# Kernel tuning notes

Hardware: AMD Instinct MI355X
Metric: run time of the kernel (lower is better)

Reference implementation:

```python
import jax, jax.numpy as jnp
import numpy as np

B, N, K = 4, 4096, 16
DP, DM = 128, 512


def _gather(points, idx):
    # points [B,N,C], idx [B,N,K] -> [B,N,K,C] (index_points)
    b, n, k = idx.shape
    flat = jnp.take_along_axis(points, idx.reshape(b, -1)[:, :, None], axis=1)
    return flat.reshape(b, n, k, points.shape[-1])


def _mlp2(x, w1, b1, w2, b2):
    return jax.nn.relu(x @ w1 + b1) @ w2 + b2


def setup_inputs():
    key = jax.random.key(0)
    ks = jax.random.split(key, 20)
    s_dp = 1.0 / np.sqrt(DP)
    s_dm = 1.0 / np.sqrt(DM)
    return {
        "xyz": jax.random.normal(ks[0], (B, N, 3), jnp.float32),
        "features": jax.random.normal(ks[1], (B, N, DP), jnp.float32),
        "fc1_w": jax.random.normal(ks[2], (DP, DM), jnp.float32) * s_dp,
        "fc1_b": jnp.zeros((DM,), jnp.float32),
        "fc2_w": jax.random.normal(ks[3], (DM, DP), jnp.float32) * s_dm,
        "fc2_b": jnp.zeros((DP,), jnp.float32),
        "wq": jax.random.normal(ks[4], (DM, DM), jnp.float32) * s_dm,
        "wk": jax.random.normal(ks[5], (DM, DM), jnp.float32) * s_dm,
        "wv": jax.random.normal(ks[6], (DM, DM), jnp.float32) * s_dm,
        "d1_w": jax.random.normal(ks[7], (3, DM), jnp.float32) * (1.0 / np.sqrt(3.0)),
        "d1_b": jnp.zeros((DM,), jnp.float32),
        "d2_w": jax.random.normal(ks[8], (DM, DM), jnp.float32) * s_dm,
        "d2_b": jnp.zeros((DM,), jnp.float32),
        "g1_w": jax.random.normal(ks[9], (DM, DM), jnp.float32) * s_dm,
        "g1_b": jnp.zeros((DM,), jnp.float32),
        "g2_w": jax.random.normal(ks[10], (DM, DM), jnp.float32) * s_dm,
        "g2_b": jnp.zeros((DM,), jnp.float32),
    }


def reference(xyz, features, fc1_w, fc1_b, fc2_w, fc2_b, wq, wk, wv,
              d1_w, d1_b, d2_w, d2_b, g1_w, g1_b, g2_w, g2_b):
    # square_distance via ||a-b||^2 = |a|^2 + |b|^2 - 2 a.b  (avoids [B,N,N,3])
    sq = jnp.sum(xyz * xyz, axis=-1)                       # [B,N]
    dists = sq[:, :, None] + sq[:, None, :] - 2.0 * jnp.einsum('bnc,bmc->bnm', xyz, xyz)
    knn_idx = jax.lax.top_k(-dists, K)[1]                  # [B,N,K] k-nearest
    knn_xyz = _gather(xyz, knn_idx)                        # [B,N,K,3]

    pre = features
    x = features @ fc1_w + fc1_b                           # [B,N,DM]
    q = x @ wq                                             # [B,N,DM]
    k = _gather(x @ wk, knn_idx)                           # [B,N,K,DM]
    v = _gather(x @ wv, knn_idx)                           # [B,N,K,DM]

    pos_enc = _mlp2(xyz[:, :, None] - knn_xyz, d1_w, d1_b, d2_w, d2_b)  # [B,N,K,DM]
    attn = _mlp2(q[:, :, None] - k + pos_enc, g1_w, g1_b, g2_w, g2_b)   # [B,N,K,DM]
    attn = jax.nn.softmax(attn / np.sqrt(DM), axis=-2)     # softmax over neighbors
    res = jnp.sum(attn * (v + pos_enc), axis=2)            # einsum bmnf,bmnf->bmf
    res = res @ fc2_w + fc2_b + pre                        # [B,N,DP]
    return res, attn
```

## Files before the change

### kernel.cpp

```cpp
#include <hip/hip_runtime.h>

#define NPTS   4096
#define NBATCH 4
#define KNN    16
#define DMODEL 512
#define DPOINT 128
#define QKVLD  1536

#define BN 128
#define BK 64

typedef unsigned short bfu;
typedef __attribute__((ext_vector_type(8))) short short8;
typedef __attribute__((ext_vector_type(4))) float f32x4;

__device__ __forceinline__ bfu f2bf(float f) {
    unsigned u = __builtin_bit_cast(unsigned, f);
    return (bfu)((u + 0x7fffu + ((u >> 16) & 1u)) >> 16);
}
__device__ __forceinline__ float bf2f(bfu h) {
    unsigned u = ((unsigned)h) << 16;
    return __builtin_bit_cast(float, u);
}

__device__ __forceinline__ void gload_lds16(const bfu* g, bfu* l) {
    __builtin_amdgcn_global_load_lds(
        (const __attribute__((address_space(1))) void*)g,
        (__attribute__((address_space(3))) void*)l, 16, 0, 0);
}

#define TPQ 8
#define QPB 32

__device__ __forceinline__ void knn_merge_level(float* bd, int* bi, int lvl)
{
    float pd[KNN]; int pi[KNN];
#pragma unroll
    for (int i = 0; i < KNN; ++i) {
        pd[i] = __shfl_xor(bd[KNN-1-i], lvl);
        pi[i] = __shfl_xor(bi[KNN-1-i], lvl);
    }
#pragma unroll
    for (int i = 0; i < KNN; ++i) {
        bool take = (pd[i] < bd[i]) || (pd[i] == bd[i] && pi[i] < bi[i]);
        if (take) { bd[i] = pd[i]; bi[i] = pi[i]; }
    }
#pragma unroll
    for (int s = 8; s >= 1; s >>= 1) {
#pragma unroll
        for (int i = 0; i < KNN; ++i) {
            if ((i & s) == 0) {
                const int j = i + s;
                bool sw = (bd[j] < bd[i]) || (bd[j] == bd[i] && bi[j] < bi[i]);
                if (sw) {
                    float td = bd[i]; bd[i] = bd[j]; bd[j] = td;
                    int   ti = bi[i]; bi[i] = bi[j]; bi[j] = ti;
                }
            }
        }
    }
}

__global__ __launch_bounds__(256) void knn_kernel(const float* __restrict__ xyz,
                                                  int* __restrict__ knn_out)
{
    __shared__ float4 pts[NPTS];
    const int b    = blockIdx.y;
    const int tid  = threadIdx.x;
    const int qloc = tid >> 3;
    const int sub  = tid & 7;
    const int n    = blockIdx.x * QPB + qloc;

    const float* bx = xyz + (size_t)b * NPTS * 3;
    for (int i = tid; i < NPTS; i += 256) {
        float x = bx[i*3+0], y = bx[i*3+1], z = bx[i*3+2];
        pts[i] = make_float4(x, y, z, x*x + y*y + z*z);
    }
    __syncthreads();

    const float4 me = pts[n];
    float bd[KNN];
    int   bi[KNN];
#pragma unroll
    for (int i = 0; i < KNN; ++i) { bd[i] = 3.4e38f; bi[i] = -1; }

    for (int t0 = 0; t0 < NPTS / TPQ; t0 += 8) {
        float d[8];
#pragma unroll
        for (int j = 0; j < 8; ++j) {
            float4 o = pts[sub + ((t0 + j) << 3)];
            d[j] = me.w + o.w - 2.f*(me.x*o.x + me.y*o.y + me.z*o.z);
        }
        float mn = fminf(fminf(fminf(d[0],d[1]),fminf(d[2],d[3])),
                         fminf(fminf(d[4],d[5]),fminf(d[6],d[7])));
        if (mn < bd[KNN-1]) {
#pragma unroll
            for (int j = 0; j < 8; ++j) {
                float dj = d[j];
                if (dj < bd[KNN-1]) {
                    const int m = sub + ((t0 + j) << 3);
#pragma unroll
                    for (int i = KNN-1; i >= 1; --i) {
                        float dp = bd[i-1];
                        if (dp > dj)        { bd[i] = dp; bi[i] = bi[i-1]; }
                        else if (bd[i] > dj){ bd[i] = dj; bi[i] = m; }
                    }
                    if (bd[0] > dj) { bd[0] = dj; bi[0] = m; }
                }
            }
        }
    }

    knn_merge_level(bd, bi, 1);
    knn_merge_level(bd, bi, 2);
    knn_merge_level(bd, bi, 4);

    int* orow = knn_out + ((size_t)b*NPTS + n) * KNN;
    const int base = b * NPTS;
    orow[sub*2+0] = base + bi[sub*2+0];
    orow[sub*2+1] = base + bi[sub*2+1];
}

__global__ __launch_bounds__(256) void prep_weights(
    const float* __restrict__ fc1_w, const float* __restrict__ wq,
    const float* __restrict__ wk,    const float* __restrict__ wv,
    const float* __restrict__ d2_w,  const float* __restrict__ g1_w,
    const float* __restrict__ g2_w,  const float* __restrict__ fc2_w,
    bfu* __restrict__ fc1T, bfu* __restrict__ qkvT, bfu* __restrict__ d2T,
    bfu* __restrict__ g1T,  bfu* __restrict__ g2T,  bfu* __restrict__ fc2T)
{
    int i = blockIdx.x * 256 + threadIdx.x;
    const int S1 = DPOINT * DMODEL;
    const int S2 = DMODEL * DMODEL;
    if (i < S1) { fc1T[i] = f2bf(fc1_w[(size_t)(i & 127) * DMODEL + (i >> 7)]); return; }
    i -= S1;
    if (i < S2) { qkvT[i]        = f2bf(wq[(size_t)(i & 511) * DMODEL + (i >> 9)]); return; }
    i -= S2;
    if (i < S2) { qkvT[S2 + i]   = f2bf(wk[(size_t)(i & 511) * DMODEL + (i >> 9)]); return; }
    i -= S2;
    if (i < S2) { qkvT[2*S2 + i] = f2bf(wv[(size_t)(i & 511) * DMODEL + (i >> 9)]); return; }
    i -= S2;
    if (i < S2) { d2T[i] = f2bf(d2_w[(size_t)(i & 511) * DMODEL + (i >> 9)]); return; }
    i -= S2;
    if (i < S2) { g1T[i] = f2bf(g1_w[(size_t)(i & 511) * DMODEL + (i >> 9)]); return; }
    i -= S2;
    if (i < S2) { g2T[i] = f2bf(g2_w[(size_t)(i & 511) * DMODEL + (i >> 9)]); return; }
    i -= S2;
    if (i < S1) { fc2T[i] = f2bf(fc2_w[(size_t)(i & 511) * DPOINT + (i >> 9)]); return; }
}

__global__ __launch_bounds__(256) void cvt_bf16(const float* __restrict__ src,
                                                bfu* __restrict__ dst, int n4)
{
    int i = blockIdx.x * 256 + threadIdx.x;
    if (i < n4) {
        float4 v = ((const float4*)src)[i];
        bfu* d = dst + (size_t)i * 4;
        d[0] = f2bf(v.x); d[1] = f2bf(v.y); d[2] = f2bf(v.z); d[3] = f2bf(v.w);
    }
}

__global__ __launch_bounds__(256) void pos_h_kernel(
    const float* __restrict__ xyz, const int* __restrict__ knng,
    const float* __restrict__ d1w, const float* __restrict__ d1b,
    bfu* __restrict__ out, int row_base)
{
    const int idx  = blockIdx.x * 256 + threadIdx.x;
    const int rloc = idx >> 6;
    const int c0   = (idx & 63) * 8;
    const int grow = row_base + rloc;
    const int p    = grow >> 4;
    const int nb   = knng[grow];
    const float rx = xyz[(size_t)p*3+0] - xyz[(size_t)nb*3+0];
    const float ry = xyz[(size_t)p*3+1] - xyz[(size_t)nb*3+1];
    const float rz = xyz[(size_t)p*3+2] - xyz[(size_t)nb*3+2];
    short8 ov;
#pragma unroll
    for (int j = 0; j < 8; ++j) {
        const int k = c0 + j;
        float v = d1b[k];
        v = fmaf(rx, d1w[k],        v);
        v = fmaf(ry, d1w[512 + k],  v);
        v = fmaf(rz, d1w[1024 + k], v);
        ov[j] = (short)f2bf(fmaxf(v, 0.f));
    }
    *(short8*)&out[(size_t)rloc * DMODEL + c0] = ov;
}

template<int BMt, bool BIAS, bool RELU, bool OUTBF, bool RESID, bool AIN, bool SMAX>
__global__ __launch_bounds__(256) void gemm_mfma(
    const bfu* __restrict__ A, const bfu* __restrict__ BT,
    const float* __restrict__ bias, const float* __restrict__ resid,
    void* __restrict__ Cout, int M, int Kd, int Nd,
    const int* __restrict__ knng,
    const bfu* __restrict__ qb, const bfu* __restrict__ kb,
    const bfu* __restrict__ posc, const bfu* __restrict__ vb,
    bfu* __restrict__ auxb, int row_base)
{
    constexpr int MF  = BMt / 32;
    constexpr int RPW = BMt / 4;

    __shared__ bfu As[BMt * BK];
    __shared__ bfu Bs[BN * BK];

    const int tid  = threadIdx.x;
    const int lane = tid & 63;
    const int w    = tid >> 6;

    const int nbn     = Nd / BN;
    const int q8      = gridDim.x >> 3;
    const int logical = (blockIdx.x & 7) * q8 + (blockIdx.x >> 3);
    const int bm      = (logical / nbn) * BMt;
    const int bn      = (logical % nbn) * BN;

    const int wm   = (w >> 1) * (BMt / 2);
    const int wn   = (w & 1) * 64;
    const int lrow = lane & 15;
    const int kgrp = lane >> 4;

    f32x4 acc[MF][4];
#pragma unroll
    for (int m = 0; m < MF; ++m)
#pragma unroll
        for (int n = 0; n < 4; ++n) acc[m][n] = (f32x4){0.f, 0.f, 0.f, 0.f};

    for (int k0 = 0; k0 < Kd; k0 += BK) {
        __syncthreads();

        {
            int r0 = w * 32;
            const bfu* gB = BT + (size_t)(bn + r0 + (lane >> 3)) * Kd + k0 + (lane & 7) * 8;
            bfu* lB = Bs + r0 * BK;
#pragma unroll
            for (int i = 0; i < 4; ++i)
                gload_lds16(gB + (size_t)i * 8 * Kd, lB + i * 8 * BK);
        }
        {
            int r0 = w * RPW;
            const bfu* gA = A + (size_t)(bm + r0 + (lane >> 3)) * Kd + k0 + (lane & 7) * 8;
            bfu* lA = As + r0 * BK;
#pragma unroll
            for (int i = 0; i < RPW / 8; ++i)
                gload_lds16(gA + (size_t)i * 8 * Kd, lA + i * 8 * BK);
        }

        __syncthreads();

#pragma unroll
        for (int kk = 0; kk < BK; kk += 32) {
            short8 af[MF], bfr[4];
#pragma unroll
            for (int m = 0; m < MF; ++m)
                af[m] = *(const short8*)&As[(wm + m * 16 + lrow) * BK + kk + kgrp * 8];
#pragma unroll
            for (int n = 0; n < 4; ++n)
                bfr[n] = *(const short8*)&Bs[(wn + n * 16 + lrow) * BK + kk + kgrp * 8];
#pragma unroll
            for (int m = 0; m < MF; ++m)
#pragma unroll
                for (int n = 0; n < 4; ++n)
                    acc[m][n] = __builtin_amdgcn_mfma_f32_16x16x32_bf16(
                        af[m], bfr[n], acc[m][n], 0, 0, 0);
        }
    }

    if constexpr (AIN) {
#pragma unroll
        for (int m = 0; m < MF; ++m) {
            const int row0 = bm + wm + m * 16 + kgrp * 4;
            int p4[4], g4[4];
#pragma unroll
            for (int r = 0; r < 4; ++r) {
                const int grow = row_base + row0 + r;
                p4[r] = grow >> 4;
                g4[r] = knng[grow];
            }
#pragma unroll
            for (int n = 0; n < 4; ++n) {
                const int col = bn + wn + n * 16 + lrow;
                const float bv = bias[col];
#pragma unroll
                for (int r = 0; r < 4; ++r) {
                    const size_t o = (size_t)(row0 + r) * DMODEL + col;
                    bfu pb = f2bf(acc[m][n][r] + bv);
                    ((bfu*)Cout)[o] = pb;
                    float qv = bf2f(qb[(size_t)p4[r] * QKVLD + col]);
                    float kv = bf2f(kb[(size_t)g4[r] * QKVLD + col]);
                    auxb[o] = f2bf(qv - kv + bf2f(pb));
                }
            }
        }
        return;
    }

    if constexpr (SMAX) {
        const float scale = 0.044194173824159216f;
#pragma unroll
        for (int m = 0; m < MF; ++m) {
            const int row0 = bm + wm + m * 16 + kgrp * 4;
            const int ploc = (bm + wm + m * 16) >> 4;
            int gnb4[4];
#pragma unroll
            for (int r = 0; r < 4; ++r) gnb4[r] = knng[(size_t)row_base + row0 + r];
#pragma unroll
            for (int n = 0; n < 4; ++n) {
                const int col = bn + wn + n * 16 + lrow;
                const float bv = bias[col];
                float v0 = (acc[m][n][0] + bv) * scale;
                float v1 = (acc[m][n][1] + bv) * scale;
                float v2 = (acc[m][n][2] + bv) * scale;
                float v3 = (acc[m][n][3] + bv) * scale;
                float mx = fmaxf(fmaxf(v0, v1), fmaxf(v2, v3));
                mx = fmaxf(mx, __shfl_xor(mx, 16));
                mx = fmaxf(mx, __shfl_xor(mx, 32));
                float e0 = __expf(v0 - mx), e1 = __expf(v1 - mx);
                float e2 = __expf(v2 - mx), e3 = __expf(v3 - mx);
                float s = e0 + e1 + e2 + e3;
                s += __shfl_xor(s, 16);
                s += __shfl_xor(s, 32);
                const float inv = 1.f / s;
                float a0 = e0*inv, a1 = e1*inv, a2 = e2*inv, a3 = e3*inv;
                float* ao = (float*)Cout;
                ao[(size_t)(row0 + 0) * DMODEL + col] = a0;
                ao[(size_t)(row0 + 1) * DMODEL + col] = a1;
                ao[(size_t)(row0 + 2) * DMODEL + col] = a2;
                ao[(size_t)(row0 + 3) * DMODEL + col] = a3;
                float res = 0.f;
                res = fmaf(a0, bf2f(vb[(size_t)gnb4[0]*QKVLD + col]) + bf2f(posc[(size_t)(row0+0)*DMODEL + col]), res);
                res = fmaf(a1, bf2f(vb[(size_t)gnb4[1]*QKVLD + col]) + bf2f(posc[(size_t)(row0+1)*DMODEL + col]), res);
                res = fmaf(a2, bf2f(vb[(size_t)gnb4[2]*QKVLD + col]) + bf2f(posc[(size_t)(row0+2)*DMODEL + col]), res);
                res = fmaf(a3, bf2f(vb[(size_t)gnb4[3]*QKVLD + col]) + bf2f(posc[(size_t)(row0+3)*DMODEL + col]), res);
                res += __shfl_xor(res, 16);
                res += __shfl_xor(res, 32);
                if (kgrp == 0) {
                    const size_t pglob = (size_t)(row_base >> 4) + ploc;
                    auxb[pglob * DMODEL + col] = f2bf(res);
                }
            }
        }
        return;
    }

#pragma unroll
    for (int m = 0; m < MF; ++m) {
#pragma unroll
        for (int n = 0; n < 4; ++n) {
            int col = bn + wn + n * 16 + lrow;
            float bv = BIAS ? bias[col] : 0.f;
#pragma unroll
            for (int r = 0; r < 4; ++r) {
                int row = bm + wm + m * 16 + kgrp * 4 + r;
                float v = acc[m][n][r] + bv;
                if (RESID) v += resid[(size_t)row * Nd + col];
                if (RELU)  v = fmaxf(v, 0.f);
                if (OUTBF) ((bfu*)Cout)[(size_t)row * Nd + col] = f2bf(v);
                else     ((float*)Cout)[(size_t)row * Nd + col] = v;
            }
        }
    }
}

extern "C" void kernel_launch(void* const* d_in, const int* in_sizes, int n_in,
                              void* d_out, int out_size, void* d_ws, size_t ws_size,
                              hipStream_t stream)
{
    const float* xyz      = (const float*)d_in[0];
    const float* features = (const float*)d_in[1];
    const float* fc1_w    = (const float*)d_in[2];
    const float* fc1_b    = (const float*)d_in[3];
    const float* fc2_w    = (const float*)d_in[4];
    const float* fc2_b    = (const float*)d_in[5];
    const float* wq       = (const float*)d_in[6];
    const float* wk       = (const float*)d_in[7];
    const float* wv       = (const float*)d_in[8];
    const float* d1_w     = (const float*)d_in[9];
    const float* d1_b     = (const float*)d_in[10];
    const float* d2_w     = (const float*)d_in[11];
    const float* d2_b     = (const float*)d_in[12];
    const float* g1_w     = (const float*)d_in[13];
    const float* g1_b     = (const float*)d_in[14];
    const float* g2_w     = (const float*)d_in[15];
    const float* g2_b     = (const float*)d_in[16];

    const size_t Mpts  = (size_t)NBATCH * NPTS;
    const size_t Mrows = Mpts * KNN;
    float* out_res  = (float*)d_out;
    float* out_attn = (float*)d_out + Mpts * DPOINT;

    size_t off = 0;
    auto ab = [&](size_t elems) { bfu* r = (bfu*)((char*)d_ws + off); off += elems * 2; return r; };
    bfu* fc1T  = ab((size_t)DMODEL * DPOINT);
    bfu* qkvT  = ab((size_t)QKVLD * DMODEL);
    bfu* d2T   = ab((size_t)DMODEL * DMODEL);
    bfu* g1T   = ab((size_t)DMODEL * DMODEL);
    bfu* g2T   = ab((size_t)DMODEL * DMODEL);
    bfu* fc2T  = ab((size_t)DPOINT * DMODEL);
    bfu* featb = ab(Mpts * DPOINT);
    bfu* xb    = ab(Mpts * DMODEL);
    bfu* qkvb  = ab(Mpts * QKVLD);
    bfu* resb  = xb;
    int* knng  = (int*)((char*)d_ws + off); off += Mrows * 4;

    int nchunk = 32;
    {
        const int cands[4] = {4, 8, 16, 32};
        for (int i = 0; i < 4; ++i) {
            size_t need = off + 3ull * (Mrows / cands[i]) * DMODEL * 2;
            if (need <= ws_size) { nchunk = cands[i]; break; }
        }
    }
    const size_t Rc  = Mrows / nchunk;
    bfu* posc = ab(Rc * DMODEL);
    bfu* hc   = ab(Rc * DMODEL);
    bfu* ainb = ab(Rc * DMODEL);

    knn_kernel<<<dim3(NPTS/QPB, NBATCH), 256, 0, stream>>>(xyz, knng);

    {
        const int total = 2 * DPOINT * DMODEL + 6 * DMODEL * DMODEL;
        prep_weights<<<dim3((total + 255) / 256), 256, 0, stream>>>(
            fc1_w, wq, wk, wv, d2_w, g1_w, g2_w, fc2_w,
            fc1T, qkvT, d2T, g1T, g2T, fc2T);
    }
    cvt_bf16<<<dim3((Mpts*DPOINT/4+255)/256), 256, 0, stream>>>(features, featb, (int)(Mpts*DPOINT/4));

#define GARGS(Ap, Bp, biasp, residp, Cp, M_, K_, N_, auxp, rb) \
    (Ap), (Bp), (biasp), (residp), (Cp), (int)(M_), (int)(K_), (int)(N_), \
    knng, qkvb, qkvb + DMODEL, posc, qkvb + 2*DMODEL, (auxp), (int)(rb)

    gemm_mfma<128, true,  false, true,  false, false, false><<<dim3((Mpts/128)*(DMODEL/BN)), 256, 0, stream>>>(
        GARGS(featb, fc1T, fc1_b, nullptr, xb, Mpts, DPOINT, DMODEL, resb, 0));
    gemm_mfma<128, false, false, true,  false, false, false><<<dim3((Mpts/128)*(QKVLD/BN)), 256, 0, stream>>>(
        GARGS(xb, qkvT, nullptr, nullptr, qkvb, Mpts, DMODEL, QKVLD, resb, 0));

    for (int c = 0; c < nchunk; ++c) {
        const size_t rb = (size_t)c * Rc;
        float* attn_c = out_attn + rb * DMODEL;

        pos_h_kernel<<<dim3((unsigned)(Rc/4)), 256, 0, stream>>>(xyz, knng, d1_w, d1_b, hc, (int)rb);

#define CHUNK_LAUNCH(BMT) \
        gemm_mfma<BMT, true, false, true, false, true, false><<<dim3((unsigned)((Rc/BMT)*(DMODEL/BN))), 256, 0, stream>>>( \
            GARGS(hc, d2T, d2_b, nullptr, posc, Rc, DMODEL, DMODEL, ainb, rb)); \
        gemm_mfma<BMT, true, true,  true, false, false, false><<<dim3((unsigned)((Rc/BMT)*(DMODEL/BN))), 256, 0, stream>>>( \
            GARGS(ainb, g1T, g1_b, nullptr, hc, Rc, DMODEL, DMODEL, resb, rb)); \
        gemm_mfma<BMT, false, false, false, false, false, true><<<dim3((unsigned)((Rc/BMT)*(DMODEL/BN))), 256, 0, stream>>>( \
            GARGS(hc, g2T, g2_b, nullptr, attn_c, Rc, DMODEL, DMODEL, resb, rb));

        if (Rc >= 32768) { CHUNK_LAUNCH(128) }
        else             { CHUNK_LAUNCH(64)  }
#undef CHUNK_LAUNCH
    }

    gemm_mfma<128, true, false, false, true, false, false><<<dim3((Mpts/128)*(DPOINT/BN)), 256, 0, stream>>>(
        GARGS(resb, fc2T, fc2_b, features, out_res, Mpts, DMODEL, DPOINT, resb, 0));
#undef GARGS
}
```

Before: 1.974 ms.

## Split KNN search across a full wavefront per query with branchless insertion

The KNN kernel now assigns 64 lanes (one wavefront) to each query instead of 8 threads, and reads points from a precomputed float4 global buffer instead of staging the whole batch in LDS. Insertion into the sorted top-16 list is made branchless, and three extra shuffle merge levels combine results across the wavefront. The aim is more parallelism per query, shorter per-thread scans, and no per-block LDS staging. In exchange every candidate pays the full 16-step insertion with no early-reject filter, there are six costly bitonic merge levels, and an extra small preprocessing kernel is launched.

```diff
diff --git a/kernel.cpp b/kernel.cpp
--- a/kernel.cpp
+++ b/kernel.cpp
@@ -29,8 +29,13 @@
         (__attribute__((address_space(3))) void*)l, 16, 0, 0);
 }
 
-#define TPQ 8
-#define QPB 32
+__global__ __launch_bounds__(256) void pts4_kernel(const float* __restrict__ xyz,
+                                                   float4* __restrict__ pts4)
+{
+    int i = blockIdx.x * 256 + threadIdx.x;
+    float x = xyz[i*3+0], y = xyz[i*3+1], z = xyz[i*3+2];
+    pts4[i] = make_float4(x, y, z, x*x + y*y + z*z);
+}
 
 __device__ __forceinline__ void knn_merge_level(float* bd, int* bi, int lvl)
 {
@@ -61,64 +66,55 @@
     }
 }
 
-__global__ __launch_bounds__(256) void knn_kernel(const float* __restrict__ xyz,
+__global__ __launch_bounds__(256) void knn_kernel(const float4* __restrict__ pts4,
                                                   int* __restrict__ knn_out)
 {
-    __shared__ float4 pts[NPTS];
     const int b    = blockIdx.y;
     const int tid  = threadIdx.x;
-    const int qloc = tid >> 3;
-    const int sub  = tid & 7;
-    const int n    = blockIdx.x * QPB + qloc;
-
-    const float* bx = xyz + (size_t)b * NPTS * 3;
-    for (int i = tid; i < NPTS; i += 256) {
-        float x = bx[i*3+0], y = bx[i*3+1], z = bx[i*3+2];
-        pts[i] = make_float4(x, y, z, x*x + y*y + z*z);
-    }
-    __syncthreads();
-
-    const float4 me = pts[n];
+    const int qloc = tid >> 6;
+    const int lane = tid & 63;
+    const int n    = blockIdx.x * 4 + qloc;
+
+    const float4* bp = pts4 + (size_t)b * NPTS;
+    const float4 me = bp[n];
     float bd[KNN];
     int   bi[KNN];
 #pragma unroll
     for (int i = 0; i < KNN; ++i) { bd[i] = 3.4e38f; bi[i] = -1; }
 
-    for (int t0 = 0; t0 < NPTS / TPQ; t0 += 8) {
-        float d[8];
-#pragma unroll
-        for (int j = 0; j < 8; ++j) {
-            float4 o = pts[sub + ((t0 + j) << 3)];
-            d[j] = me.w + o.w - 2.f*(me.x*o.x + me.y*o.y + me.z*o.z);
-        }
-        float mn = fminf(fminf(fminf(d[0],d[1]),fminf(d[2],d[3])),
-                         fminf(fminf(d[4],d[5]),fminf(d[6],d[7])));
-        if (mn < bd[KNN-1]) {
-#pragma unroll
-            for (int j = 0; j < 8; ++j) {
-                float dj = d[j];
-                if (dj < bd[KNN-1]) {
-                    const int m = sub + ((t0 + j) << 3);
-#pragma unroll
-                    for (int i = KNN-1; i >= 1; --i) {
-                        float dp = bd[i-1];
-                        if (dp > dj)        { bd[i] = dp; bi[i] = bi[i-1]; }
-                        else if (bd[i] > dj){ bd[i] = dj; bi[i] = m; }
-                    }
-                    if (bd[0] > dj) { bd[0] = dj; bi[0] = m; }
-                }
-            }
+    for (int t0 = 0; t0 < NPTS / 64; t0 += 4) {
+#pragma unroll
+        for (int j = 0; j < 4; ++j) {
+            const int m = lane + ((t0 + j) << 6);
+            float4 o = bp[m];
+            const float dj = me.w + o.w - 2.f*(me.x*o.x + me.y*o.y + me.z*o.z);
+#pragma unroll
+            for (int i = KNN-1; i >= 1; --i) {
+                const float dp = bd[i-1];
+                const int   ip = bi[i-1];
+                const bool shift = dp    > dj;
+                const bool repl  = bd[i] > dj;
+                bd[i] = shift ? dp : (repl ? dj : bd[i]);
+                bi[i] = shift ? ip : (repl ? m  : bi[i]);
+            }
+            const bool r0 = bd[0] > dj;
+            bd[0] = r0 ? dj : bd[0];
+            bi[0] = r0 ? m  : bi[0];
         }
     }
 
     knn_merge_level(bd, bi, 1);
     knn_merge_level(bd, bi, 2);
     knn_merge_level(bd, bi, 4);
+    knn_merge_level(bd, bi, 8);
+    knn_merge_level(bd, bi, 16);
+    knn_merge_level(bd, bi, 32);
 
     int* orow = knn_out + ((size_t)b*NPTS + n) * KNN;
-    const int base = b * NPTS;
-    orow[sub*2+0] = base + bi[sub*2+0];
-    orow[sub*2+1] = base + bi[sub*2+1];
+    int v = bi[0];
+#pragma unroll
+    for (int i = 1; i < KNN; ++i) if (lane == i) v = bi[i];
+    if (lane < KNN) orow[lane] = b * NPTS + v;
 }
 
 __global__ __launch_bounds__(256) void prep_weights(
@@ -389,6 +385,7 @@
 
     size_t off = 0;
     auto ab = [&](size_t elems) { bfu* r = (bfu*)((char*)d_ws + off); off += elems * 2; return r; };
+    float4* pts4 = (float4*)d_ws; off += Mpts * sizeof(float4);
     bfu* fc1T  = ab((size_t)DMODEL * DPOINT);
     bfu* qkvT  = ab((size_t)QKVLD * DMODEL);
     bfu* d2T   = ab((size_t)DMODEL * DMODEL);
@@ -414,7 +411,8 @@
     bfu* hc   = ab(Rc * DMODEL);
     bfu* ainb = ab(Rc * DMODEL);
 
-    knn_kernel<<<dim3(NPTS/QPB, NBATCH), 256, 0, stream>>>(xyz, knng);
+    pts4_kernel<<<dim3(Mpts/256), 256, 0, stream>>>(xyz, pts4);
+    knn_kernel<<<dim3(NPTS/4, NBATCH), 256, 0, stream>>>(pts4, knng);
 
     {
         const int total = 2 * DPOINT * DMODEL + 6 * DMODEL * DMODEL;
```

Measured after the change: 2.342 ms. +18.6%, slower.
